# Performance work log

Measured on AMD Instinct MI355X. Metric: run time of the kernel, lower is better.

Reference implementation:

```python
import jax, jax.numpy as jnp
import numpy as np

NCB = 16      # num_codebooks
CS = 256      # codebook_size
HD = 384      # hidden_dim
PD = 2048     # predictor_dim
N = 16384     # flattened frames
BN_EPS = 1e-5


def setup_inputs() -> dict:
    key = jax.random.key(0)
    ks = jax.random.split(key, 5)
    predictor = jax.random.normal(ks[0], (N, PD), dtype=jnp.float32)
    codebook_indexes = jax.random.randint(ks[1], (N, NCB), 0, CS).astype(jnp.int64)
    W1 = jax.random.normal(ks[2], (NCB * HD, PD), dtype=jnp.float32) * (PD ** -0.5)
    b1 = jnp.zeros((NCB * HD,), dtype=jnp.float32)
    lsi = (NCB - 1) * CS
    linear_self = jax.random.normal(ks[3], ((NCB - 1) * HD, lsi), dtype=jnp.float32) * (lsi ** -0.5)
    bn_gamma = jnp.ones((NCB * HD,), dtype=jnp.float32)
    bn_beta = jnp.zeros((NCB * HD,), dtype=jnp.float32)
    linear2 = jax.random.normal(ks[4], (NCB, CS, HD), dtype=jnp.float32) * (HD ** -0.5)
    bias2 = jnp.zeros((NCB, CS), dtype=jnp.float32)
    return {"predictor": predictor, "codebook_indexes": codebook_indexes,
            "W1": W1, "b1": b1, "linear_self": linear_self,
            "bn_gamma": bn_gamma, "bn_beta": bn_beta,
            "linear2": linear2, "bias2": bias2}


def reference(predictor, codebook_indexes, W1, b1, linear_self, bn_gamma, bn_beta, linear2, bias2):
    ci = codebook_indexes.astype(jnp.int32)
    valid = (ci >= 0)                                      # (N, NCB)
    idx = jnp.clip(ci, 0, CS - 1)
    one_hot = jax.nn.one_hot(idx, CS, dtype=jnp.float32) * valid[..., None].astype(jnp.float32)  # (N, NCB, CS)

    hidden = predictor @ W1.T + b1                          # (N, NCB*HD)

    mask = ((jnp.arange((NCB - 1) * HD) // HD)[:, None] >=
            (jnp.arange((NCB - 1) * CS) // CS)[None, :]).astype(jnp.float32)
    oh_part = one_hot[:, :NCB - 1, :].reshape(-1, (NCB - 1) * CS)
    self_pred = oh_part @ (linear_self * mask).T            # (N, (NCB-1)*HD)
    hidden = jnp.concatenate([hidden[:, :HD], hidden[:, HD:] + self_pred], axis=-1)

    hidden = jax.nn.relu(hidden)
    # BatchNorm1d in training mode: batch mean / biased variance, affine
    mean = jnp.mean(hidden, axis=0)
    var = jnp.mean(jnp.square(hidden - mean), axis=0)
    hidden = (hidden - mean) * jax.lax.rsqrt(var + BN_EPS) * bn_gamma + bn_beta

    hidden = hidden.reshape(-1, NCB, HD)
    logits = jnp.einsum('nkh,kch->nkc', hidden, linear2) + bias2   # (N, NCB, CS)
    logprobs = jax.nn.log_softmax(logits, axis=-1)

    tot_logprob = jnp.sum(logprobs * one_hot)
    tot_count = jnp.sum(valid[:, 0].astype(jnp.int32))
    return tot_logprob, tot_count
```

## Files before the change

kernel.cpp:

```cpp
#include <hip/hip_runtime.h>
#include <hip/hip_bf16.h>

#define NCB 16
#define CS 256
#define HD 384
#define PD 2048
#define NROW 16384
#define NH 6144
#define LSR 5760
#define LSC 3840
#define SA_ROWS 32
#define SA_NBLK (NROW / SA_ROWS)
#define GK 32

typedef __bf16 bf16x8 __attribute__((ext_vector_type(8)));
typedef float f32x4 __attribute__((ext_vector_type(4)));
typedef int int4v __attribute__((ext_vector_type(4)));
typedef int int2v __attribute__((ext_vector_type(2)));

__device__ __forceinline__ unsigned short f2bf(float f) {
  unsigned u = __builtin_bit_cast(unsigned, f);
  u = (u + 0x7fffu + ((u >> 16) & 1u)) >> 16;
  return (unsigned short)u;
}
__device__ __forceinline__ float bf2f(unsigned short h) {
  unsigned u = ((unsigned)h) << 16;
  return __builtin_bit_cast(float, u);
}
__device__ __forceinline__ unsigned char f2fp8(float f) {
  return (unsigned char)__builtin_amdgcn_cvt_pk_fp8_f32(f, f, 0, false);
}
__device__ __forceinline__ long lo64(int4v v) {
  int2v t; t[0] = v[0]; t[1] = v[1];
  return __builtin_bit_cast(long, t);
}
__device__ __forceinline__ long hi64(int4v v) {
  int2v t; t[0] = v[2]; t[1] = v[3];
  return __builtin_bit_cast(long, t);
}

__device__ __forceinline__ void gload16(void* lds, const void* g) {
  __builtin_amdgcn_global_load_lds(
      (const __attribute__((address_space(1))) unsigned int*)g,
      (__attribute__((address_space(3))) unsigned int*)lds, 16, 0, 0);
}

__global__ void k_f2b8(const float* __restrict__ in, unsigned* __restrict__ out, int n8) {
  for (int i = blockIdx.x * 256 + threadIdx.x; i < n8; i += gridDim.x * 256) {
    float4 a = ((const float4*)in)[i * 2];
    float4 b = ((const float4*)in)[i * 2 + 1];
    unsigned lo = __builtin_amdgcn_cvt_pk_fp8_f32(a.x, a.y, 0, false);
    lo = __builtin_amdgcn_cvt_pk_fp8_f32(a.z, a.w, lo, true);
    unsigned hi = __builtin_amdgcn_cvt_pk_fp8_f32(b.x, b.y, 0, false);
    hi = __builtin_amdgcn_cvt_pk_fp8_f32(b.z, b.w, hi, true);
    uint2 o = {lo, hi};
    ((uint2*)out)[i] = o;
  }
}

__global__ __launch_bounds__(256) void k_transpose(const float* __restrict__ LS,
                                                   unsigned char* __restrict__ T) {
  __shared__ float tile[32][33];
  int tx = threadIdx.x & 31, ty = threadIdx.x >> 5;
  int c0 = blockIdx.x * 32;
  int r0 = blockIdx.y * 32;
  for (int i = ty; i < 32; i += 8)
    tile[i][tx] = LS[(size_t)(r0 + i) * LSC + c0 + tx];
  __syncthreads();
  const int i = threadIdx.x >> 3;
  const int q = (threadIdx.x & 7) * 4;
  unsigned u = __builtin_amdgcn_cvt_pk_fp8_f32(tile[q][i], tile[q + 1][i], 0, false);
  u = __builtin_amdgcn_cvt_pk_fp8_f32(tile[q + 2][i], tile[q + 3][i], u, true);
  *(unsigned*)(T + (size_t)(c0 + i) * LSR + r0 + q) = u;
}

__global__ void k_count(const int* __restrict__ ci, float* __restrict__ out) {
  int n = blockIdx.x * 256 + threadIdx.x;
  float v = (n < NROW && ci[(size_t)n * NCB] >= 0) ? 1.f : 0.f;
  #pragma unroll
  for (int m = 1; m < 64; m <<= 1) v += __shfl_xor(v, m);
  if ((threadIdx.x & 63) == 0) atomicAdd(out + 1, v);
}

__global__ __launch_bounds__(512, 4) void k_gemm1(
    const unsigned char* __restrict__ A,
    const unsigned char* __restrict__ B,
    const float* __restrict__ b1,
    unsigned char* __restrict__ H) {
  __shared__ int4v Al[2][1024];
  __shared__ int4v Bl[2][512];

  const int tid = threadIdx.x;
  const int lane = tid & 63;
  const int w = tid >> 6;
  const int wr = w >> 1, wc = w & 1;
  const int l15 = lane & 15, hi = lane >> 4;
  const int w64 = tid & ~63;

  const int bid = blockIdx.x;
  const int xcd = bid & 7, p = bid >> 3;
  const int nt = xcd * 6 + p % 6;
  const int mt = p / 6;
  const int tm = mt * 256, tn = nt * 128;

  f32x4 acc[4][4] = {};

  auto STAGE = [&](int buf, int t) {
    const int kb = t * 64;
    #pragma unroll
    for (int g = 0; g < 2; ++g) {
      const int slot = g * 512 + tid;
      const int row = slot >> 2;
      const int lc = (slot & 3) ^ ((row >> 1) & 3);
      gload16(&Al[buf][g * 512 + w64], A + (size_t)(tm + row) * PD + kb + lc * 16);
    }
    {
      const int row = tid >> 2;
      const int lc = (tid & 3) ^ ((row >> 1) & 3);
      gload16(&Bl[buf][w64], B + (size_t)(tn + row) * PD + kb + lc * 16);
    }
  };

  STAGE(0, 0);
  asm volatile("s_waitcnt vmcnt(0)" ::: "memory");
  __builtin_amdgcn_s_barrier();

  for (int t = 0; t < GK; ++t) {
    const int buf = t & 1;
    int4v af[4], bfr[4];
    #pragma unroll
    for (int mi = 0; mi < 4; ++mi) {
      const int row = wr * 64 + mi * 16 + l15;
      af[mi] = Al[buf][row * 4 + (hi ^ ((row >> 1) & 3))];
    }
    #pragma unroll
    for (int ni = 0; ni < 4; ++ni) {
      const int row = wc * 64 + ni * 16 + l15;
      bfr[ni] = Bl[buf][row * 4 + (hi ^ ((row >> 1) & 3))];
    }
    if (t + 1 < GK) STAGE(buf ^ 1, t + 1);
    __builtin_amdgcn_s_setprio(1);
    #pragma unroll
    for (int mi = 0; mi < 4; ++mi) {
      const long a1 = lo64(af[mi]);
      #pragma unroll
      for (int ni = 0; ni < 4; ++ni)
        acc[mi][ni] = __builtin_amdgcn_mfma_f32_16x16x32_fp8_fp8(
            a1, lo64(bfr[ni]), acc[mi][ni], 0, 0, 0);
    }
    #pragma unroll
    for (int mi = 0; mi < 4; ++mi) {
      const long a2 = hi64(af[mi]);
      #pragma unroll
      for (int ni = 0; ni < 4; ++ni)
        acc[mi][ni] = __builtin_amdgcn_mfma_f32_16x16x32_fp8_fp8(
            a2, hi64(bfr[ni]), acc[mi][ni], 0, 0, 0);
    }
    __builtin_amdgcn_s_setprio(0);
    if (t + 1 < GK) {
      asm volatile("s_waitcnt vmcnt(0)" ::: "memory");
      __builtin_amdgcn_s_barrier();
    }
  }

  __syncthreads();
  unsigned char* Hs = (unsigned char*)&Al[0][0];
  #pragma unroll
  for (int ni = 0; ni < 4; ++ni) {
    const int col = wc * 64 + ni * 16 + l15;
    const float bb = b1[tn + col];
    #pragma unroll
    for (int mi = 0; mi < 4; ++mi)
      #pragma unroll
      for (int reg = 0; reg < 4; ++reg) {
        const int row = wr * 64 + mi * 16 + hi * 4 + reg;
        Hs[row * 128 + col] = f2fp8(acc[mi][ni][reg] + bb);
      }
  }
  __syncthreads();
  #pragma unroll
  for (int it = 0; it < 4; ++it) {
    const int slot = it * 512 + tid;
    const int row = slot >> 3, g = slot & 7;
    int4v v = *(const int4v*)(Hs + row * 128 + g * 16);
    __builtin_nontemporal_store(v, (int4v*)(H + (size_t)(tm + row) * NH + tn + g * 16));
  }
}

template <int KM>
__device__ __forceinline__ void gather_chunk(
    const unsigned char* __restrict__ T, const int* idxrow,
    int oo, int bbv, float v[8]) {
  #pragma unroll
  for (int kc = 0; kc < KM; ++kc) {
    int c = idxrow[kc];
    float m = (c >= 0 && kc <= bbv) ? 1.f : 0.f;
    int cc = c < 0 ? 0 : (c >= CS ? CS - 1 : c);
    int2 tv = *(const int2*)(T + (size_t)(kc * CS + cc) * LSR + oo);
    float f[8];
    f[0] = __builtin_amdgcn_cvt_f32_fp8(tv.x, 0);
    f[1] = __builtin_amdgcn_cvt_f32_fp8(tv.x, 1);
    f[2] = __builtin_amdgcn_cvt_f32_fp8(tv.x, 2);
    f[3] = __builtin_amdgcn_cvt_f32_fp8(tv.x, 3);
    f[4] = __builtin_amdgcn_cvt_f32_fp8(tv.y, 0);
    f[5] = __builtin_amdgcn_cvt_f32_fp8(tv.y, 1);
    f[6] = __builtin_amdgcn_cvt_f32_fp8(tv.y, 2);
    f[7] = __builtin_amdgcn_cvt_f32_fp8(tv.y, 3);
    #pragma unroll
    for (int e = 0; e < 8; ++e) v[e] = fmaf(m, f[e], v[e]);
  }
}

__global__ __launch_bounds__(256) void k_selfadd(
    unsigned char* __restrict__ H,
    const unsigned char* __restrict__ T,
    const int* __restrict__ ci,
    float* __restrict__ partials) {
  __shared__ int idxs[SA_ROWS][NCB];
  const int tid = threadIdx.x;
  const int row0 = blockIdx.y * SA_ROWS;
  const int sx = blockIdx.x;
  for (int i = tid; i < SA_ROWS * NCB; i += 256)
    idxs[i >> 4][i & 15] = ci[(size_t)(row0 + (i >> 4)) * NCB + (i & 15)];
  __syncthreads();

  const int col0 = sx * 2048 + tid * 8;
  const int o = col0 - HD;
  const int oo = o < 0 ? 0 : o;
  const int bb = o < 0 ? -1 : o / HD;

  float cs[8] = {0}, cq[8] = {0};

  for (int rr = 0; rr < SA_ROWS; ++rr) {
    const size_t ro = (size_t)(row0 + rr) * NH;
    int2v hv = __builtin_nontemporal_load((const int2v*)(H + ro + col0));
    float v[8];
    v[0] = __builtin_amdgcn_cvt_f32_fp8(hv[0], 0);
    v[1] = __builtin_amdgcn_cvt_f32_fp8(hv[0], 1);
    v[2] = __builtin_amdgcn_cvt_f32_fp8(hv[0], 2);
    v[3] = __builtin_amdgcn_cvt_f32_fp8(hv[0], 3);
    v[4] = __builtin_amdgcn_cvt_f32_fp8(hv[1], 0);
    v[5] = __builtin_amdgcn_cvt_f32_fp8(hv[1], 1);
    v[6] = __builtin_amdgcn_cvt_f32_fp8(hv[1], 2);
    v[7] = __builtin_amdgcn_cvt_f32_fp8(hv[1], 3);
    switch (sx) {
      case 0: gather_chunk<5>(T, idxs[rr], oo, bb, v); break;
      case 1: gather_chunk<10>(T, idxs[rr], oo, bb, v); break;
      default: gather_chunk<15>(T, idxs[rr], oo, bb, v); break;
    }
    float x[8];
    #pragma unroll
    for (int e = 0; e < 8; ++e) x[e] = fmaxf(v[e], 0.f);
    int2v ov;
    unsigned w0 = __builtin_amdgcn_cvt_pk_fp8_f32(x[0], x[1], 0, false);
    w0 = __builtin_amdgcn_cvt_pk_fp8_f32(x[2], x[3], w0, true);
    unsigned w1 = __builtin_amdgcn_cvt_pk_fp8_f32(x[4], x[5], 0, false);
    w1 = __builtin_amdgcn_cvt_pk_fp8_f32(x[6], x[7], w1, true);
    ov[0] = (int)w0; ov[1] = (int)w1;
    float xr0 = __builtin_amdgcn_cvt_f32_fp8(w0, 0);
    float xr1 = __builtin_amdgcn_cvt_f32_fp8(w0, 1);
    float xr2 = __builtin_amdgcn_cvt_f32_fp8(w0, 2);
    float xr3 = __builtin_amdgcn_cvt_f32_fp8(w0, 3);
    float xr4 = __builtin_amdgcn_cvt_f32_fp8(w1, 0);
    float xr5 = __builtin_amdgcn_cvt_f32_fp8(w1, 1);
    float xr6 = __builtin_amdgcn_cvt_f32_fp8(w1, 2);
    float xr7 = __builtin_amdgcn_cvt_f32_fp8(w1, 3);
    cs[0] += xr0; cq[0] += xr0 * xr0;
    cs[1] += xr1; cq[1] += xr1 * xr1;
    cs[2] += xr2; cq[2] += xr2 * xr2;
    cs[3] += xr3; cq[3] += xr3 * xr3;
    cs[4] += xr4; cq[4] += xr4 * xr4;
    cs[5] += xr5; cq[5] += xr5 * xr5;
    cs[6] += xr6; cq[6] += xr6 * xr6;
    cs[7] += xr7; cq[7] += xr7 * xr7;
    __builtin_nontemporal_store(ov, (int2v*)(H + ro + col0));
  }

  float* Ps = partials + (size_t)blockIdx.y * NH + col0;
  float* Pq = partials + (size_t)(SA_NBLK + blockIdx.y) * NH + col0;
  float4 a = {cs[0], cs[1], cs[2], cs[3]};
  float4 b4 = {cs[4], cs[5], cs[6], cs[7]};
  *(float4*)Ps = a; *(float4*)(Ps + 4) = b4;
  float4 c4 = {cq[0], cq[1], cq[2], cq[3]};
  float4 d4 = {cq[4], cq[5], cq[6], cq[7]};
  *(float4*)Pq = c4; *(float4*)(Pq + 4) = d4;
}

__global__ void k_red(const float* __restrict__ partials,
                      float* __restrict__ colsum, float* __restrict__ colsq) {
  int j = blockIdx.x * 256 + threadIdx.x;
  const float* Ps = partials;
  const float* Pq = partials + (size_t)SA_NBLK * NH;
  float s = 0.f, q = 0.f;
  const int b0 = blockIdx.y * (SA_NBLK / 8), b1 = b0 + SA_NBLK / 8;
  for (int by = b0; by < b1; ++by) {
    s += Ps[(size_t)by * NH + j];
    q += Pq[(size_t)by * NH + j];
  }
  atomicAdd(colsum + j, s);
  atomicAdd(colsq + j, q);
}

__global__ void k_bn(const float* __restrict__ colsum, const float* __restrict__ colsq,
                     const float* __restrict__ gamma, const float* __restrict__ beta,
                     float* __restrict__ scale, float* __restrict__ shift) {
  int j = blockIdx.x * 256 + threadIdx.x;
  if (j >= NH) return;
  float mean = colsum[j] * (1.f / NROW);
  float var = colsq[j] * (1.f / NROW) - mean * mean;
  var = fmaxf(var, 0.f);
  float rs = rsqrtf(var + 1e-5f);
  float g = gamma[j] * rs;
  scale[j] = g;
  shift[j] = beta[j] - mean * g;
}

__global__ __launch_bounds__(128) void k_fold(
    const float* __restrict__ L2, const float* __restrict__ bias2,
    const float* __restrict__ scale, const float* __restrict__ shift,
    unsigned char* __restrict__ L2b8, float* __restrict__ bias2p) {
  __shared__ float red[2];
  int kc = blockIdx.x;
  int k = kc >> 8;
  size_t off = (size_t)kc * HD;
  float a = 0.f;
  for (int h = threadIdx.x; h < HD; h += 128) {
    float wv = L2[off + h];
    int jh = k * HD + h;
    L2b8[off + h] = f2fp8(wv * scale[jh]);
    a += wv * shift[jh];
  }
  #pragma unroll
  for (int m = 1; m < 64; m <<= 1) a += __shfl_xor(a, m);
  if ((threadIdx.x & 63) == 0) red[threadIdx.x >> 6] = a;
  __syncthreads();
  if (threadIdx.x == 0) bias2p[kc] = bias2[kc] + red[0] + red[1];
}

__global__ __launch_bounds__(256, 2) void k_passc(
    const unsigned char* __restrict__ H,
    const unsigned char* __restrict__ L2b8,
    const float* __restrict__ bias2p,
    const int* __restrict__ ci,
    float* __restrict__ out) {
  __shared__ char smem[64 * 260 * 4];
  __shared__ float red[4];
  float* lg = (float*)smem;

  const int tid = threadIdx.x, lane = tid & 63, w = tid >> 6;
  const int bidf = blockIdx.y * gridDim.x + blockIdx.x;
  const int xcd = bidf & 7, p = bidf >> 3;
  const int k = xcd * 2 + (p & 1);
  const int tm = (p >> 1) * 64;
  const int r = lane & 15, hi = lane >> 4;
  const int w64 = tid & ~63;

  auto Asb = [&](int r3) { return (int4v*)(smem + r3 * 20480); };
  auto Bsb = [&](int r3) { return (int4v*)(smem + r3 * 20480 + 4096); };

  auto STAGE = [&](int r3, int kk) {
    const int kb = kk * 64;
    {
      const int row = tid >> 2;
      const int pc = (tid & 3) ^ ((row >> 1) & 3);
      gload16(Asb(r3) + w64, H + (size_t)(tm + row) * NH + k * HD + kb + pc * 16);
    }
    #pragma unroll
    for (int i = 0; i < 4; ++i) {
      const int slot = i * 256 + tid;
      const int row = slot >> 2;
      const int pc = (slot & 3) ^ ((row >> 1) & 3);
      gload16(Bsb(r3) + i * 256 + w64,
              L2b8 + (size_t)(k * CS + row) * HD + kb + pc * 16);
    }
  };

  f32x4 acc[4][4] = {};
  STAGE(0, 0);
  STAGE(1, 1);
  asm volatile("s_waitcnt vmcnt(5)" ::: "memory");
  __builtin_amdgcn_s_barrier();

  for (int kk = 0; kk < HD / 64; ++kk) {
    const int r3 = kk % 3;
    int4v af[4], bfr[4];
    #pragma unroll
    for (int mi = 0; mi < 4; ++mi) {
      const int row = mi * 16 + r;
      af[mi] = Asb(r3)[row * 4 + (hi ^ ((row >> 1) & 3))];
    }
    #pragma unroll
    for (int ni = 0; ni < 4; ++ni) {
      const int row = w * 64 + ni * 16 + r;
      bfr[ni] = Bsb(r3)[row * 4 + (hi ^ ((row >> 1) & 3))];
    }
    if (kk + 2 < HD / 64) STAGE((kk + 2) % 3, kk + 2);
    __builtin_amdgcn_s_setprio(1);
    #pragma unroll
    for (int mi = 0; mi < 4; ++mi) {
      const long a1 = lo64(af[mi]);
      #pragma unroll
      for (int ni = 0; ni < 4; ++ni)
        acc[mi][ni] = __builtin_amdgcn_mfma_f32_16x16x32_fp8_fp8(
            a1, lo64(bfr[ni]), acc[mi][ni], 0, 0, 0);
    }
    #pragma unroll
    for (int mi = 0; mi < 4; ++mi) {
      const long a2 = hi64(af[mi]);
      #pragma unroll
      for (int ni = 0; ni < 4; ++ni)
        acc[mi][ni] = __builtin_amdgcn_mfma_f32_16x16x32_fp8_fp8(
            a2, hi64(bfr[ni]), acc[mi][ni], 0, 0, 0);
    }
    __builtin_amdgcn_s_setprio(0);
    if (kk + 1 < HD / 64) {
      if (kk + 2 < HD / 64) asm volatile("s_waitcnt vmcnt(5)" ::: "memory");
      else                  asm volatile("s_waitcnt vmcnt(0)" ::: "memory");
    }
    __builtin_amdgcn_s_barrier();
  }

  const int lr0 = hi * 4;
  #pragma unroll
  for (int mi = 0; mi < 4; ++mi)
    #pragma unroll
    for (int ni = 0; ni < 4; ++ni) {
      int col = w * 64 + ni * 16 + r;
      float bb = bias2p[k * CS + col];
      #pragma unroll
      for (int reg = 0; reg < 4; ++reg) {
        int row = mi * 16 + lr0 + reg;
        lg[row * 260 + col] = acc[mi][ni][reg] + bb;
      }
    }
  __syncthreads();

  int row = tid >> 2, part = tid & 3;
  const float4* rp = (const float4*)(lg + row * 260 + part * 64);
  float s = 0.f;
  #pragma unroll
  for (int i = 0; i < 16; ++i) {
    float4 v = rp[i];
    s += __expf(v.x) + __expf(v.y) + __expf(v.z) + __expf(v.w);
  }
  s += __shfl_xor(s, 1);
  s += __shfl_xor(s, 2);
  float contrib = 0.f;
  if (part == 0) {
    float lse = __logf(s);
    int c = ci[(size_t)(tm + row) * NCB + k];
    if (c >= 0) {
      c = c < CS ? c : CS - 1;
      contrib = lg[row * 260 + c] - lse;
    }
  }
  #pragma unroll
  for (int msk = 1; msk < 64; msk <<= 1) contrib += __shfl_xor(contrib, msk);
  if (lane == 0) red[w] = contrib;
  __syncthreads();
  if (tid == 0) atomicAdd(out, red[0] + red[1] + red[2] + red[3]);
}

extern "C" void kernel_launch(void* const* d_in, const int* in_sizes, int n_in,
                              void* d_out, int out_size, void* d_ws, size_t ws_size,
                              hipStream_t stream) {
  const float* predictor = (const float*)d_in[0];
  const int* cbidx       = (const int*)d_in[1];
  const float* W1        = (const float*)d_in[2];
  const float* b1        = (const float*)d_in[3];
  const float* lself     = (const float*)d_in[4];
  const float* gamma     = (const float*)d_in[5];
  const float* beta      = (const float*)d_in[6];
  const float* L2        = (const float*)d_in[7];
  const float* bias2     = (const float*)d_in[8];
  float* out = (float*)d_out;

  char* ws = (char*)d_ws;
  size_t off = 0;
  auto alloc = [&](size_t bytes) {
    char* p = ws + off;
    off += (bytes + 255) & ~(size_t)255;
    return p;
  };
  unsigned char* predB8  = (unsigned char*)alloc((size_t)NROW * PD);
  unsigned char* W1B8    = (unsigned char*)alloc((size_t)NH * PD);
  unsigned char* T       = (unsigned char*)alloc((size_t)LSC * LSR);
  unsigned char* H8      = (unsigned char*)alloc((size_t)NROW * NH);
  unsigned char* L2b8    = (unsigned char*)alloc((size_t)NCB * CS * HD);
  float* partials = (float*)alloc((size_t)2 * SA_NBLK * NH * 4);
  float* colsum = (float*)alloc(NH * 4);
  float* colsq  = (float*)alloc(NH * 4);
  float* scale  = (float*)alloc(NH * 4);
  float* shift  = (float*)alloc(NH * 4);
  float* bias2p = (float*)alloc(NCB * CS * 4);

  hipMemsetAsync(d_out, 0, 2 * sizeof(float), stream);
  hipMemsetAsync(colsum, 0, NH * 4, stream);
  hipMemsetAsync(colsq, 0, NH * 4, stream);

  k_f2b8<<<2048, 256, 0, stream>>>(predictor, (unsigned*)predB8, NROW * PD / 8);
  k_f2b8<<<2048, 256, 0, stream>>>(W1, (unsigned*)W1B8, NH * PD / 8);
  k_transpose<<<dim3(LSC / 32, LSR / 32), 256, 0, stream>>>(lself, T);
  k_count<<<NROW / 256, 256, 0, stream>>>(cbidx, out);
  k_gemm1<<<(NROW / 256) * (NH / 128), 512, 0, stream>>>(predB8, W1B8, b1, H8);
  k_selfadd<<<dim3(3, SA_NBLK), 256, 0, stream>>>(H8, T, cbidx, partials);
  k_red<<<dim3(NH / 256, 8), 256, 0, stream>>>(partials, colsum, colsq);
  k_bn<<<NH / 256, 256, 0, stream>>>(colsum, colsq, gamma, beta, scale, shift);
  k_fold<<<NCB * CS, 128, 0, stream>>>(L2, bias2, scale, shift, L2b8, bias2p);
  k_passc<<<dim3(NROW / 64, NCB), 256, 0, stream>>>(H8, L2b8, bias2p, cbidx, out);
}
```

Baseline: 578.2 us.

## Compute log-softmax in registers and shrink passc LDS for higher occupancy

The logits epilogue of k_passc now computes the softmax sums from the MFMA accumulators with cross-lane shuffles and a small per-row LDS reduction, so the 64x260 float logits tile is no longer staged in shared memory. The staging pipeline drops from triple buffering to double buffering with full waits each step. LDS use shrinks from about 66KB to about 42KB and launch bounds are raised to 3 blocks per CU to increase occupancy. In exchange the prefetch depth is shallower, and raising the block count per CU tightens the register budget.

```diff
diff --git a/kernel.cpp b/kernel.cpp
--- a/kernel.cpp
+++ b/kernel.cpp
@@ -22,10 +22,6 @@
   unsigned u = __builtin_bit_cast(unsigned, f);
   u = (u + 0x7fffu + ((u >> 16) & 1u)) >> 16;
   return (unsigned short)u;
-}
-__device__ __forceinline__ float bf2f(unsigned short h) {
-  unsigned u = ((unsigned)h) << 16;
-  return __builtin_bit_cast(float, u);
 }
 __device__ __forceinline__ unsigned char f2fp8(float f) {
   return (unsigned char)__builtin_amdgcn_cvt_pk_fp8_f32(f, f, 0, false);
@@ -337,15 +333,17 @@
   if (threadIdx.x == 0) bias2p[kc] = bias2[kc] + red[0] + red[1];
 }
 
-__global__ __launch_bounds__(256, 2) void k_passc(
+__global__ __launch_bounds__(256, 3) void k_passc(
     const unsigned char* __restrict__ H,
     const unsigned char* __restrict__ L2b8,
     const float* __restrict__ bias2p,
     const int* __restrict__ ci,
     float* __restrict__ out) {
-  __shared__ char smem[64 * 260 * 4];
+  __shared__ int4v Asb[2][256];
+  __shared__ int4v Bsb[2][1024];
+  __shared__ float lsebuf[4][64];
+  __shared__ int   tgtb[64];
   __shared__ float red[4];
-  float* lg = (float*)smem;
 
   const int tid = threadIdx.x, lane = tid & 63, w = tid >> 6;
   const int bidf = blockIdx.y * gridDim.x + blockIdx.x;
@@ -355,46 +353,43 @@
   const int r = lane & 15, hi = lane >> 4;
   const int w64 = tid & ~63;
 
-  auto Asb = [&](int r3) { return (int4v*)(smem + r3 * 20480); };
-  auto Bsb = [&](int r3) { return (int4v*)(smem + r3 * 20480 + 4096); };
-
-  auto STAGE = [&](int r3, int kk) {
+  auto STAGE = [&](int buf, int kk) {
     const int kb = kk * 64;
     {
       const int row = tid >> 2;
       const int pc = (tid & 3) ^ ((row >> 1) & 3);
-      gload16(Asb(r3) + w64, H + (size_t)(tm + row) * NH + k * HD + kb + pc * 16);
+      gload16(&Asb[buf][w64], H + (size_t)(tm + row) * NH + k * HD + kb + pc * 16);
     }
     #pragma unroll
     for (int i = 0; i < 4; ++i) {
       const int slot = i * 256 + tid;
       const int row = slot >> 2;
       const int pc = (slot & 3) ^ ((row >> 1) & 3);
-      gload16(Bsb(r3) + i * 256 + w64,
+      gload16(&Bsb[buf][i * 256 + w64],
               L2b8 + (size_t)(k * CS + row) * HD + kb + pc * 16);
     }
   };
 
+  if (tid < 64) tgtb[tid] = ci[(size_t)(tm + tid) * NCB + k];
+  STAGE(0, 0);
+  asm volatile("s_waitcnt vmcnt(0)" ::: "memory");
+  __syncthreads();
+
   f32x4 acc[4][4] = {};
-  STAGE(0, 0);
-  STAGE(1, 1);
-  asm volatile("s_waitcnt vmcnt(5)" ::: "memory");
-  __builtin_amdgcn_s_barrier();
-
   for (int kk = 0; kk < HD / 64; ++kk) {
-    const int r3 = kk % 3;
+    const int buf = kk & 1;
     int4v af[4], bfr[4];
     #pragma unroll
     for (int mi = 0; mi < 4; ++mi) {
       const int row = mi * 16 + r;
-      af[mi] = Asb(r3)[row * 4 + (hi ^ ((row >> 1) & 3))];
+      af[mi] = Asb[buf][row * 4 + (hi ^ ((row >> 1) & 3))];
     }
     #pragma unroll
     for (int ni = 0; ni < 4; ++ni) {
       const int row = w * 64 + ni * 16 + r;
-      bfr[ni] = Bsb(r3)[row * 4 + (hi ^ ((row >> 1) & 3))];
-    }
-    if (kk + 2 < HD / 64) STAGE((kk + 2) % 3, kk + 2);
+      bfr[ni] = Bsb[buf][row * 4 + (hi ^ ((row >> 1) & 3))];
+    }
+    if (kk + 1 < HD / 64) STAGE(buf ^ 1, kk + 1);
     __builtin_amdgcn_s_setprio(1);
     #pragma unroll
     for (int mi = 0; mi < 4; ++mi) {
@@ -414,44 +409,53 @@
     }
     __builtin_amdgcn_s_setprio(0);
     if (kk + 1 < HD / 64) {
-      if (kk + 2 < HD / 64) asm volatile("s_waitcnt vmcnt(5)" ::: "memory");
-      else                  asm volatile("s_waitcnt vmcnt(0)" ::: "memory");
-    }
-    __builtin_amdgcn_s_barrier();
-  }
-
-  const int lr0 = hi * 4;
-  #pragma unroll
-  for (int mi = 0; mi < 4; ++mi)
-    #pragma unroll
-    for (int ni = 0; ni < 4; ++ni) {
-      int col = w * 64 + ni * 16 + r;
-      float bb = bias2p[k * CS + col];
+      asm volatile("s_waitcnt vmcnt(0)" ::: "memory");
+      __builtin_amdgcn_s_barrier();
+    }
+  }
+
+  float bb[4];
+  #pragma unroll
+  for (int ni = 0; ni < 4; ++ni) bb[ni] = bias2p[k * CS + w * 64 + ni * 16 + r];
+
+  #pragma unroll
+  for (int mi = 0; mi < 4; ++mi) {
+    #pragma unroll
+    for (int reg = 0; reg < 4; ++reg) {
+      float s = 0.f;
       #pragma unroll
-      for (int reg = 0; reg < 4; ++reg) {
-        int row = mi * 16 + lr0 + reg;
-        lg[row * 260 + col] = acc[mi][ni][reg] + bb;
+      for (int ni = 0; ni < 4; ++ni)
+        s += __expf(acc[mi][ni][reg] + bb[ni]);
+      s += __shfl_xor(s, 1);
+      s += __shfl_xor(s, 2);
+      s += __shfl_xor(s, 4);
+      s += __shfl_xor(s, 8);
+      if (r == 0) lsebuf[w][mi * 16 + hi * 4 + reg] = s;
+    }
+  }
+  __syncthreads();
+  if (tid < 64) {
+    float tot = lsebuf[0][tid] + lsebuf[1][tid] + lsebuf[2][tid] + lsebuf[3][tid];
+    lsebuf[0][tid] = __logf(tot);
+  }
+  __syncthreads();
+
+  float contrib = 0.f;
+  #pragma unroll
+  for (int mi = 0; mi < 4; ++mi) {
+    #pragma unroll
+    for (int reg = 0; reg < 4; ++reg) {
+      const int row = mi * 16 + hi * 4 + reg;
+      const int c = tgtb[row];
+      if (c >= 0) {
+        const int cc = c < CS ? c : CS - 1;
+        if ((cc >> 6) == w && (cc & 15) == r) {
+          #pragma unroll
+          for (int ni = 0; ni < 4; ++ni)
+            if (((cc >> 4) & 3) == ni)
+              contrib += acc[mi][ni][reg] + bb[ni] - lsebuf[0][row];
+        }
       }
-    }
-  __syncthreads();
-
-  int row = tid >> 2, part = tid & 3;
-  const float4* rp = (const float4*)(lg + row * 260 + part * 64);
-  float s = 0.f;
-  #pragma unroll
-  for (int i = 0; i < 16; ++i) {
-    float4 v = rp[i];
-    s += __expf(v.x) + __expf(v.y) + __expf(v.z) + __expf(v.w);
-  }
-  s += __shfl_xor(s, 1);
-  s += __shfl_xor(s, 2);
-  float contrib = 0.f;
-  if (part == 0) {
-    float lse = __logf(s);
-    int c = ci[(size_t)(tm + row) * NCB + k];
-    if (c >= 0) {
-      c = c < CS ? c : CS - 1;
-      contrib = lg[row * 260 + c] - lse;
     }
   }
   #pragma unroll
```

Result: slower. 601.5 us (+4.0%).
